# Kernel tuning notes

Hardware: AMD Instinct MI355X
Metric: run time of the kernel (lower is better)

The kernel has to match this reference:

```python
import jax, jax.numpy as jnp
import numpy as np

TEMP = 0.1
TEMP_SUP = 0.5
PROP = 0.5  # proportion_pure_contrastive
SIGMA = 1.0
GAMMA = 1.0 / (2.0 * SIGMA ** 2)
INF = 1e8


def _l2norm(x, eps=1e-12):
    # torch F.normalize: x / max(||x||, eps)
    n = jnp.sqrt(jnp.sum(x * x, axis=-1, keepdims=True))
    return x / jnp.maximum(n, eps)


def _cross_entropy(logits, targets):
    # mean over rows of -log_softmax(logits)[i, targets[i]]
    logp = jax.nn.log_softmax(logits, axis=-1)
    return -jnp.mean(jnp.take_along_axis(logp, targets[:, None], axis=-1))


def setup_inputs() -> dict:
    key = jax.random.key(0)
    k1, k2, k3 = jax.random.split(key, 3)
    N, D = 4096, 256
    z_i = jax.random.normal(k1, (N, D), dtype=jnp.float32)
    z_j = jax.random.normal(k2, (N, D), dtype=jnp.float32)
    labels = jax.random.normal(k3, (N, 1), dtype=jnp.float32)
    return {"z_i": z_i, "z_j": z_j, "labels": labels}


def _forward(z_i, z_j, labels):
    N = z_i.shape[0]
    eye = jnp.eye(N, dtype=z_i.dtype)
    zin = _l2norm(z_i)
    zjn = _l2norm(z_j)

    # ---- pure contrastive branch (temperature TEMP) ----
    sim_zii = zin @ zin.T / TEMP - INF * eye
    sim_zjj = zjn @ zjn.T / TEMP - INF * eye
    sim_zij = zin @ zjn.T / TEMP
    correct = jnp.arange(N, dtype=jnp.int32)
    loss_i = _cross_entropy(jnp.concatenate([sim_zij, sim_zii], axis=1), correct)
    loss_j = _cross_entropy(jnp.concatenate([sim_zij.T, sim_zjj], axis=1), correct)
    loss_pure = loss_i + loss_j

    # ---- supervised branch (temperature TEMP_SUP) ----
    s_zii = zin @ zin.T / TEMP_SUP - INF * eye
    s_zjj = zjn @ zjn.T / TEMP_SUP - INF * eye
    s_zij = zin @ zjn.T / TEMP_SUP

    # RBF kernel on duplicated labels (detached in original -> stop_gradient)
    all_lab = jnp.tile(labels.reshape(N, -1), (2, 1))  # [2N, L]
    all_lab = jax.lax.stop_gradient(all_lab)
    sq = jnp.sum(all_lab * all_lab, axis=1)
    d2 = sq[:, None] + sq[None, :] - 2.0 * (all_lab @ all_lab.T)
    weights = jnp.exp(-GAMMA * jnp.maximum(d2, 0.0))  # [2N, 2N]
    weights = weights * (1.0 - jnp.eye(2 * N, dtype=weights.dtype))
    norm = jnp.sum(weights, axis=1, keepdims=True)  # [2N, 1]
    weights = weights / norm
    weights_norm = weights * jnp.log(norm)

    sim_Z = jnp.concatenate([
        jnp.concatenate([s_zii, s_zij], axis=1),
        jnp.concatenate([s_zij.T, s_zjj], axis=1),
    ], axis=0)  # [2N, 2N]
    log_sim_Z = jax.nn.log_softmax(sim_Z, axis=1)
    loss_sup = (-1.0 / N) * jnp.sum(weights * log_sim_Z)
    loss_sup += (-1.0 / N) * jnp.sum(weights_norm)

    return PROP * loss_pure + (1.0 - PROP) * loss_sup


def reference(z_i, z_j, labels):
    return _forward(z_i, z_j, labels)
```

## Files before the change

kernel.cpp:

```cpp
#include <hip/hip_runtime.h>
#include <hip/hip_bf16.h>

#define NN 4096
#define DD 256
#define CCN 8
#define TPB 16
#define LOG2E 1.44269504088896f

typedef __attribute__((ext_vector_type(8))) short bf16x8;
typedef __attribute__((ext_vector_type(4))) float f32x4;
typedef __attribute__((ext_vector_type(2))) float f32x2;

typedef const unsigned int __attribute__((address_space(1)))* gu32p;
typedef unsigned int __attribute__((address_space(3)))* su32p;

__device__ __forceinline__ float fexp2(float x) { return __builtin_amdgcn_exp2f(x); }

__global__ __launch_bounds__(256) void k_norm(const float* __restrict__ zi,
                                              const float* __restrict__ zj,
                                              const float* __restrict__ labels,
                                              __hip_bfloat16* __restrict__ oi,
                                              __hip_bfloat16* __restrict__ oj,
                                              float* __restrict__ T,
                                              float* __restrict__ out) {
  if (blockIdx.x == 0 && threadIdx.x == 0) out[0] = 0.f;
  int gw = (blockIdx.x * 256 + threadIdx.x) >> 6;
  int lane = threadIdx.x & 63;
  int wave = threadIdx.x >> 6;
  const float* src = (gw < NN) ? zi : zj;
  __hip_bfloat16* dst = (gw < NN) ? oi : oj;
  int row = (gw < NN) ? gw : gw - NN;
  float4 v = ((const float4*)(src + (size_t)row * DD))[lane];
  float ss = v.x * v.x + v.y * v.y + v.z * v.z + v.w * v.w;
#pragma unroll
  for (int m = 1; m < 64; m <<= 1) ss += __shfl_xor(ss, m);
  float s = 1.0f / fmaxf(sqrtf(ss), 1e-12f);
  __hip_bfloat16* d = dst + (size_t)row * DD + lane * 4;
  d[0] = __float2bfloat16(v.x * s);
  d[1] = __float2bfloat16(v.y * s);
  d[2] = __float2bfloat16(v.z * s);
  d[3] = __float2bfloat16(v.w * s);

  if (wave < 2) {
    int r = blockIdx.x * 2 + wave;
    float lr = labels[r];
    float acc = 0.f;
    for (int it = 0; it < NN / 64; ++it) {
      float dl = lr - labels[it * 64 + lane];
      acc += fexp2(dl * dl * (-0.5f * LOG2E));
    }
#pragma unroll
    for (int m = 1; m < 64; m <<= 1) acc += __shfl_xor(acc, m);
    if (lane == 0) T[r] = acc;
  }
}

template <int MODE, bool COL>
__device__ __forceinline__ void epi(
    const f32x4 acc[2][2], const f32x2 labr[2][2], const float* __restrict__ labels,
    f32x2 rA[2][2], f32x2 rB[2][2], f32x2 rC[2][2],
    float cw[2][3], float* __restrict__ diag,
    int rowbase, int colbase, int wave, int fr, int kg) {
#pragma unroll
  for (int cf = 0; cf < 2; ++cf) {
    const int cg = colbase + cf * 16 + fr;
    const float labc = labels[cg];
    const f32x2 labc2 = {labc, labc};
#pragma unroll
    for (int sub = 0; sub < 2; ++sub) {
#pragma unroll
      for (int pp = 0; pp < 2; ++pp) {
        f32x2 S = {acc[sub][cf][2 * pp], acc[sub][cf][2 * pp + 1]};
        f32x2 arg = S * (2.f * LOG2E) + (-2.f * LOG2E);
        f32x2 b;
        b.x = fexp2(arg.x);
        b.y = fexp2(arg.y);
        f32x2 b2 = b * b;
        f32x2 b5 = b2 * b2 * b;
        f32x2 dl = labr[sub][pp] - labc2;
        f32x2 e = (dl * (-0.5f * LOG2E)) * dl;
        f32x2 kk;
        kk.x = fexp2(e.x);
        kk.y = fexp2(e.y);
        f32x2 ks = kk * S;
        if (MODE != 0) {
          const int rg = rowbase + wave * 32 + sub * 16 + kg * 4 + 2 * pp;
          if (MODE == 1) {
            if (rg == cg) diag[cg] = S.x;
            if (rg + 1 == cg) diag[cg] = S.y;
          } else {
            if (rg == cg)     { b5.x = 0.f; b.x = 0.f; ks.x = 0.f; }
            if (rg + 1 == cg) { b5.y = 0.f; b.y = 0.f; ks.y = 0.f; }
          }
        }
        rA[sub][pp] += b5;
        rB[sub][pp] += b;
        rC[sub][pp] += ks;
        if (COL) {
          cw[cf][0] += b5.x + b5.y;
          cw[cf][1] += b.x + b.y;
          cw[cf][2] += ks.x + ks.y;
        }
      }
    }
  }
}

__global__ __launch_bounds__(256, 2) void k_main(
    const __hip_bfloat16* __restrict__ zin, const __hip_bfloat16* __restrict__ zjn,
    const float* __restrict__ labels,
    float* __restrict__ part, float* __restrict__ colp, float* __restrict__ diag) {
  __shared__ short lB[2][32 * 256];
  __shared__ float colw[2][4][3][32];

  const int cc = blockIdx.x;
  const int by = blockIdx.y;
  const int combo = blockIdx.z;
  const bool COLF = (combo == 0);

  const __hip_bfloat16* Ap = (combo == 2) ? zjn : zin;
  const __hip_bfloat16* Bp = (combo == 1) ? zin : zjn;

  const int tid = threadIdx.x;
  const int lane = tid & 63;
  const int wave = tid >> 6;
  const int fr = lane & 15;
  const int kg = lane >> 4;
  const int rowbase = by * 128;
  char* lBc = (char*)lB;

  bf16x8 a[2][8];
#pragma unroll
  for (int sub = 0; sub < 2; ++sub) {
    const __hip_bfloat16* Ar =
        Ap + (size_t)(rowbase + wave * 32 + sub * 16 + fr) * DD + kg * 8;
#pragma unroll
    for (int k = 0; k < 8; ++k) a[sub][k] = *(const bf16x8*)(Ar + k * 32);
  }

  f32x2 labr[2][2];
#pragma unroll
  for (int sub = 0; sub < 2; ++sub)
#pragma unroll
    for (int pp = 0; pp < 2; ++pp) {
      const float* lp = labels + rowbase + wave * 32 + sub * 16 + kg * 4 + 2 * pp;
      labr[sub][pp] = (f32x2){lp[0], lp[1]};
    }

  f32x2 rA[2][2] = {}, rB[2][2] = {}, rC[2][2] = {};

  const int frb = (fr >> 2) & 1;
  const int P0 = fr * 512 + ((kg ^ (fr & 3)) << 4) + (frb << 6);

#define STAGE(t, buf)                                                         \
  {                                                                           \
    const char* Bt = (const char*)Bp + (size_t)(cc * 512 + (t) * 32) * 512;   \
    char* dst = lBc + (buf) * 16384;                                          \
    _Pragma("unroll") for (int j = 0; j < 4; ++j) {                           \
      int f = tid + 256 * j;                                                  \
      int g = f ^ ((f >> 5) & 7);                                             \
      __builtin_amdgcn_global_load_lds(                                       \
          (gu32p)(const void*)(Bt + (size_t)g * 16),                          \
          (su32p)(void*)(dst + (wave * 64 + 256 * j) * 16), 16, 0, 0);        \
    }                                                                         \
  }

  STAGE(0, 0);

  for (int t = 0; t < TPB; ++t) {
    __syncthreads();
    if (t < TPB - 1) STAGE(t + 1, (t + 1) & 1);

    if (COLF && t > 0 && tid < 96) {
      int p = tid >> 5, c = tid & 31;
      const float (*cwsrc)[3][32] = colw[(t - 1) & 1];
      float v = cwsrc[0][p][c] + cwsrc[1][p][c] + cwsrc[2][p][c] + cwsrc[3][p][c];
      colp[((size_t)(by * 128 + cc * TPB + t - 1)) * 96 + p * 32 + c] = v;
    }

    f32x4 acc[2][2];
#pragma unroll
    for (int s2 = 0; s2 < 2; ++s2)
#pragma unroll
      for (int cf = 0; cf < 2; ++cf) acc[s2][cf] = (f32x4){0.f, 0.f, 0.f, 0.f};

    const char* cur = lBc + (t & 1) * 16384;
#pragma unroll
    for (int k = 0; k < 8; ++k) {
      const char* bbase = cur + (P0 ^ (k << 6));
#pragma unroll
      for (int cf = 0; cf < 2; ++cf) {
        bf16x8 bv = *(const bf16x8*)(bbase + cf * 8192);
        acc[0][cf] = __builtin_amdgcn_mfma_f32_16x16x32_bf16(a[0][k], bv, acc[0][cf], 0, 0, 0);
        acc[1][cf] = __builtin_amdgcn_mfma_f32_16x16x32_bf16(a[1][k], bv, acc[1][cf], 0, 0, 0);
      }
    }

    const int colbase = cc * 512 + t * 32;
    const unsigned dtt = (unsigned)(t + 16 * cc - 4 * by);
    float cw[2][3] = {};
    if (COLF) {
      if (dtt < 4u)
        epi<1, true>(acc, labr, labels, rA, rB, rC, cw, diag, rowbase, colbase, wave, fr, kg);
      else
        epi<0, true>(acc, labr, labels, rA, rB, rC, cw, diag, rowbase, colbase, wave, fr, kg);
#pragma unroll
      for (int cf = 0; cf < 2; ++cf)
#pragma unroll
        for (int p = 0; p < 3; ++p) {
          float v = cw[cf][p];
          v += __shfl_xor(v, 16);
          v += __shfl_xor(v, 32);
          if (kg == 0) colw[t & 1][wave][p][cf * 16 + fr] = v;
        }
    } else {
      if (dtt < 4u)
        epi<2, false>(acc, labr, labels, rA, rB, rC, cw, diag, rowbase, colbase, wave, fr, kg);
      else
        epi<0, false>(acc, labr, labels, rA, rB, rC, cw, diag, rowbase, colbase, wave, fr, kg);
    }
  }

  if (COLF) {
    __syncthreads();
    if (tid < 96) {
      int p = tid >> 5, c = tid & 31;
      const float (*cwsrc)[3][32] = colw[(TPB - 1) & 1];
      float v = cwsrc[0][p][c] + cwsrc[1][p][c] + cwsrc[2][p][c] + cwsrc[3][p][c];
      colp[((size_t)(by * 128 + cc * TPB + TPB - 1)) * 96 + p * 32 + c] = v;
    }
  }

  float* pc = part + (size_t)cc * 9 * NN;
  const int pr = combo;
#pragma unroll
  for (int sub = 0; sub < 2; ++sub)
#pragma unroll
    for (int pp = 0; pp < 2; ++pp)
#pragma unroll
      for (int comp = 0; comp < 2; ++comp) {
        float va = rA[sub][pp][comp], vb = rB[sub][pp][comp], vc = rC[sub][pp][comp];
#pragma unroll
        for (int m = 1; m < 16; m <<= 1) {
          va += __shfl_xor(va, m);
          vb += __shfl_xor(vb, m);
          vc += __shfl_xor(vc, m);
        }
        if (fr == 0) {
          int r = rowbase + wave * 32 + sub * 16 + kg * 4 + 2 * pp + comp;
          pc[pr * NN + r] = va;
          pc[(3 + pr) * NN + r] = vb;
          pc[(6 + pr) * NN + r] = vc;
        }
      }
}

__global__ __launch_bounds__(256) void k_final(
    const float* __restrict__ part, const float* __restrict__ colp,
    const float* __restrict__ diag, const float* __restrict__ T,
    float* __restrict__ out) {
  int r = blockIdx.x * 256 + threadIdx.x;
  float st[9];
#pragma unroll
  for (int p = 0; p < 9; ++p) {
    float s = 0.f;
#pragma unroll
    for (int c = 0; c < CCN; ++c) s += part[((size_t)c * 9 + p) * NN + r];
    st[p] = s;
  }
  float a3 = 0.f, b3 = 0.f, c3 = 0.f;
  const int cct = r >> 5, c31 = r & 31;
  for (int by = 0; by < 32; ++by) {
    const float* cp = colp + ((size_t)(by * 128 + cct)) * 96;
    a3 += cp[c31];
    b3 += cp[32 + c31];
    c3 += cp[64 + c31];
  }
  float d = diag[r];
  float accP = logf(st[0] + st[1]) + logf(a3 + st[2]) + 20.f - 20.f * d;
  float nrm = 2.f * T[r] - 1.f;
  float W = 2.f * (st[6] + st[7] + c3 + st[8]) / nrm;
  float accS = logf(st[3] + st[4]) + logf(b3 + st[5]) + 4.f - W - 2.f * logf(nrm);
  float v = accP + accS;
#pragma unroll
  for (int m = 1; m < 64; m <<= 1) v += __shfl_xor(v, m);
  __shared__ float red[4];
  if ((threadIdx.x & 63) == 0) red[threadIdx.x >> 6] = v;
  __syncthreads();
  if (threadIdx.x == 0)
    atomicAdd(out, 0.5f * (red[0] + red[1] + red[2] + red[3]) / (float)NN);
}

extern "C" void kernel_launch(void* const* d_in, const int* in_sizes, int n_in,
                              void* d_out, int out_size, void* d_ws, size_t ws_size,
                              hipStream_t stream) {
  const float* zi = (const float*)d_in[0];
  const float* zj = (const float*)d_in[1];
  const float* labels = (const float*)d_in[2];
  float* out = (float*)d_out;

  char* ws = (char*)d_ws;
  __hip_bfloat16* zinH = (__hip_bfloat16*)ws;
  __hip_bfloat16* zjnH = (__hip_bfloat16*)(ws + (size_t)NN * DD * 2);
  float* part = (float*)(ws + (size_t)NN * DD * 4);
  float* colp = part + (size_t)CCN * 9 * NN;
  float* diag = colp + (size_t)4096 * 96;
  float* T = diag + NN;

  k_norm<<<2 * NN / 4, 256, 0, stream>>>(zi, zj, labels, zinH, zjnH, T, out);

  dim3 grid(CCN, NN / 128, 3);
  k_main<<<grid, 256, 0, stream>>>(zinH, zjnH, labels, part, colp, diag);

  k_final<<<NN / 256, 256, 0, stream>>>(part, colp, diag, T, out);
}
```

Measured before the change: 76.84 us.

## Read B tiles directly from global memory and drop LDS staging and barriers

The main GEMM kernel no longer stages B tiles into shared memory with async global-to-LDS copies and double buffering. Each lane now loads its B fragments straight from global memory (relying on cache), and the per-iteration __syncthreads is removed. Column partial sums are written per wave to global memory, with the final kernel reducing over four waves, instead of being combined through LDS. The launch-bounds occupancy hint is also dropped. This removes block-wide barriers and LDS traffic, but adds uncoalesced global loads, more colp writes, and a larger workspace and final-kernel read.

```diff
diff --git a/kernel.cpp b/kernel.cpp
--- a/kernel.cpp
+++ b/kernel.cpp
@@ -10,9 +10,6 @@
 typedef __attribute__((ext_vector_type(8))) short bf16x8;
 typedef __attribute__((ext_vector_type(4))) float f32x4;
 typedef __attribute__((ext_vector_type(2))) float f32x2;
-
-typedef const unsigned int __attribute__((address_space(1)))* gu32p;
-typedef unsigned int __attribute__((address_space(3)))* su32p;
 
 __device__ __forceinline__ float fexp2(float x) { return __builtin_amdgcn_exp2f(x); }
 
@@ -59,7 +56,7 @@
 __device__ __forceinline__ void epi(
     const f32x4 acc[2][2], const f32x2 labr[2][2], const float* __restrict__ labels,
     f32x2 rA[2][2], f32x2 rB[2][2], f32x2 rC[2][2],
-    float cw[2][3], float* __restrict__ diag,
+    f32x2 cw2[2][3], float* __restrict__ diag,
     int rowbase, int colbase, int wave, int fr, int kg) {
 #pragma unroll
   for (int cf = 0; cf < 2; ++cf) {
@@ -97,22 +94,19 @@
         rB[sub][pp] += b;
         rC[sub][pp] += ks;
         if (COL) {
-          cw[cf][0] += b5.x + b5.y;
-          cw[cf][1] += b.x + b.y;
-          cw[cf][2] += ks.x + ks.y;
+          cw2[cf][0] += b5;
+          cw2[cf][1] += b;
+          cw2[cf][2] += ks;
         }
       }
     }
   }
 }
 
-__global__ __launch_bounds__(256, 2) void k_main(
+__global__ __launch_bounds__(256) void k_main(
     const __hip_bfloat16* __restrict__ zin, const __hip_bfloat16* __restrict__ zjn,
     const float* __restrict__ labels,
     float* __restrict__ part, float* __restrict__ colp, float* __restrict__ diag) {
-  __shared__ short lB[2][32 * 256];
-  __shared__ float colw[2][4][3][32];
-
   const int cc = blockIdx.x;
   const int by = blockIdx.y;
   const int combo = blockIdx.z;
@@ -127,7 +121,6 @@
   const int fr = lane & 15;
   const int kg = lane >> 4;
   const int rowbase = by * 128;
-  char* lBc = (char*)lB;
 
   bf16x8 a[2][8];
 #pragma unroll
@@ -149,34 +142,10 @@
 
   f32x2 rA[2][2] = {}, rB[2][2] = {}, rC[2][2] = {};
 
-  const int frb = (fr >> 2) & 1;
-  const int P0 = fr * 512 + ((kg ^ (fr & 3)) << 4) + (frb << 6);
-
-#define STAGE(t, buf)                                                         \
-  {                                                                           \
-    const char* Bt = (const char*)Bp + (size_t)(cc * 512 + (t) * 32) * 512;   \
-    char* dst = lBc + (buf) * 16384;                                          \
-    _Pragma("unroll") for (int j = 0; j < 4; ++j) {                           \
-      int f = tid + 256 * j;                                                  \
-      int g = f ^ ((f >> 5) & 7);                                             \
-      __builtin_amdgcn_global_load_lds(                                       \
-          (gu32p)(const void*)(Bt + (size_t)g * 16),                          \
-          (su32p)(void*)(dst + (wave * 64 + 256 * j) * 16), 16, 0, 0);        \
-    }                                                                         \
-  }
-
-  STAGE(0, 0);
+  const char* Bb = (const char*)Bp + ((size_t)cc * 512) * 512 + fr * 512 + kg * 16;
 
   for (int t = 0; t < TPB; ++t) {
-    __syncthreads();
-    if (t < TPB - 1) STAGE(t + 1, (t + 1) & 1);
-
-    if (COLF && t > 0 && tid < 96) {
-      int p = tid >> 5, c = tid & 31;
-      const float (*cwsrc)[3][32] = colw[(t - 1) & 1];
-      float v = cwsrc[0][p][c] + cwsrc[1][p][c] + cwsrc[2][p][c] + cwsrc[3][p][c];
-      colp[((size_t)(by * 128 + cc * TPB + t - 1)) * 96 + p * 32 + c] = v;
-    }
+    const char* bt = Bb + (size_t)t * 16384;
 
     f32x4 acc[2][2];
 #pragma unroll
@@ -184,50 +153,39 @@
 #pragma unroll
       for (int cf = 0; cf < 2; ++cf) acc[s2][cf] = (f32x4){0.f, 0.f, 0.f, 0.f};
 
-    const char* cur = lBc + (t & 1) * 16384;
 #pragma unroll
     for (int k = 0; k < 8; ++k) {
-      const char* bbase = cur + (P0 ^ (k << 6));
-#pragma unroll
-      for (int cf = 0; cf < 2; ++cf) {
-        bf16x8 bv = *(const bf16x8*)(bbase + cf * 8192);
-        acc[0][cf] = __builtin_amdgcn_mfma_f32_16x16x32_bf16(a[0][k], bv, acc[0][cf], 0, 0, 0);
-        acc[1][cf] = __builtin_amdgcn_mfma_f32_16x16x32_bf16(a[1][k], bv, acc[1][cf], 0, 0, 0);
-      }
+      bf16x8 b0 = *(const bf16x8*)(bt + k * 64);
+      bf16x8 b1 = *(const bf16x8*)(bt + 8192 + k * 64);
+      acc[0][0] = __builtin_amdgcn_mfma_f32_16x16x32_bf16(a[0][k], b0, acc[0][0], 0, 0, 0);
+      acc[1][0] = __builtin_amdgcn_mfma_f32_16x16x32_bf16(a[1][k], b0, acc[1][0], 0, 0, 0);
+      acc[0][1] = __builtin_amdgcn_mfma_f32_16x16x32_bf16(a[0][k], b1, acc[0][1], 0, 0, 0);
+      acc[1][1] = __builtin_amdgcn_mfma_f32_16x16x32_bf16(a[1][k], b1, acc[1][1], 0, 0, 0);
     }
 
     const int colbase = cc * 512 + t * 32;
     const unsigned dtt = (unsigned)(t + 16 * cc - 4 * by);
-    float cw[2][3] = {};
+    f32x2 cw2[2][3] = {};
     if (COLF) {
       if (dtt < 4u)
-        epi<1, true>(acc, labr, labels, rA, rB, rC, cw, diag, rowbase, colbase, wave, fr, kg);
+        epi<1, true>(acc, labr, labels, rA, rB, rC, cw2, diag, rowbase, colbase, wave, fr, kg);
       else
-        epi<0, true>(acc, labr, labels, rA, rB, rC, cw, diag, rowbase, colbase, wave, fr, kg);
+        epi<0, true>(acc, labr, labels, rA, rB, rC, cw2, diag, rowbase, colbase, wave, fr, kg);
+      float* cp = colp + ((size_t)(by * 128 + cc * TPB + t) * 4 + wave) * 96;
 #pragma unroll
       for (int cf = 0; cf < 2; ++cf)
 #pragma unroll
         for (int p = 0; p < 3; ++p) {
-          float v = cw[cf][p];
+          float v = cw2[cf][p].x + cw2[cf][p].y;
           v += __shfl_xor(v, 16);
           v += __shfl_xor(v, 32);
-          if (kg == 0) colw[t & 1][wave][p][cf * 16 + fr] = v;
+          if (kg == 0) cp[p * 32 + cf * 16 + fr] = v;
         }
     } else {
       if (dtt < 4u)
-        epi<2, false>(acc, labr, labels, rA, rB, rC, cw, diag, rowbase, colbase, wave, fr, kg);
+        epi<2, false>(acc, labr, labels, rA, rB, rC, cw2, diag, rowbase, colbase, wave, fr, kg);
       else
-        epi<0, false>(acc, labr, labels, rA, rB, rC, cw, diag, rowbase, colbase, wave, fr, kg);
-    }
-  }
-
-  if (COLF) {
-    __syncthreads();
-    if (tid < 96) {
-      int p = tid >> 5, c = tid & 31;
-      const float (*cwsrc)[3][32] = colw[(TPB - 1) & 1];
-      float v = cwsrc[0][p][c] + cwsrc[1][p][c] + cwsrc[2][p][c] + cwsrc[3][p][c];
-      colp[((size_t)(by * 128 + cc * TPB + TPB - 1)) * 96 + p * 32 + c] = v;
+        epi<0, false>(acc, labr, labels, rA, rB, rC, cw2, diag, rowbase, colbase, wave, fr, kg);
     }
   }
 
@@ -271,10 +229,13 @@
   float a3 = 0.f, b3 = 0.f, c3 = 0.f;
   const int cct = r >> 5, c31 = r & 31;
   for (int by = 0; by < 32; ++by) {
-    const float* cp = colp + ((size_t)(by * 128 + cct)) * 96;
-    a3 += cp[c31];
-    b3 += cp[32 + c31];
-    c3 += cp[64 + c31];
+    const float* cp = colp + (size_t)(by * 128 + cct) * 4 * 96;
+#pragma unroll
+    for (int w = 0; w < 4; ++w) {
+      a3 += cp[w * 96 + c31];
+      b3 += cp[w * 96 + 32 + c31];
+      c3 += cp[w * 96 + 64 + c31];
+    }
   }
   float d = diag[r];
   float accP = logf(st[0] + st[1]) + logf(a3 + st[2]) + 20.f - 20.f * d;
@@ -304,7 +265,7 @@
   __hip_bfloat16* zjnH = (__hip_bfloat16*)(ws + (size_t)NN * DD * 2);
   float* part = (float*)(ws + (size_t)NN * DD * 4);
   float* colp = part + (size_t)CCN * 9 * NN;
-  float* diag = colp + (size_t)4096 * 96;
+  float* diag = colp + (size_t)4096 * 4 * 96;
   float* T = diag + NN;
 
   k_norm<<<2 * NN / 4, 256, 0, stream>>>(zi, zj, labels, zinH, zjnH, T, out);
```

Result: slower. 165.6 us (+115.5%).
